# Performance work log

Hardware: AMD Instinct MI355X
Metric: run time of the kernel (lower is better)

## Reference

```python
import jax, jax.numpy as jnp
import numpy as np


def setup_inputs() -> dict:
    key = jax.random.key(0)
    kx, ky = jax.random.split(key)
    x = jax.random.normal(kx, (16, 4096, 3), dtype=jnp.float32)
    y = jax.random.normal(ky, (16, 4096, 3), dtype=jnp.float32)
    return {"x": x, "y": y}


def reference(x, y):
    # avoiding the O(b*N*M*d) difference tensor of the naive expansion.
    x2 = jnp.sum(x * x, axis=-1)                  # (b, N)
    y2 = jnp.sum(y * y, axis=-1)                  # (b, M)
    xy = jnp.einsum('bnd,bmd->bnm', x, y)         # (b, N, M)
    dist = x2[:, :, None] + y2[:, None, :] - 2.0 * xy
    min_d = jnp.min(dist, axis=2)                 # top-1 smallest over M -> (b, N)
    chamfer = jnp.sum(min_d, axis=1) / x.shape[1] # (b,)
    return jnp.sum(chamfer)
```

## Files before the change

### kernel.cpp

```cpp
#include <hip/hip_runtime.h>


constexpr int NPTS    = 4096;
constexpr int NBATCH  = 16;
constexpr int BLOCK   = 256;
constexpr int XPT     = 4;
constexpr int XCHUNK  = BLOCK * XPT;
constexpr int YTILE   = 512;
constexpr int NXC     = NPTS / XCHUNK;
constexpr int NYC     = NPTS / YTILE;

__global__ __launch_bounds__(BLOCK) void chamfer_min_kernel(
    const float* __restrict__ x, const float* __restrict__ y,
    unsigned int* __restrict__ ws_min)
{
    __shared__ float4 sy4[YTILE * 3 / 4];

    const int b      = blockIdx.x >> 5;
    const int xchunk = (blockIdx.x >> 3) & (NXC - 1);
    const int ychunk = blockIdx.x & (NYC - 1);

    const float4* yb4 = (const float4*)(y + ((size_t)b * NPTS + ychunk * YTILE) * 3);
    for (int i = threadIdx.x; i < YTILE * 3 / 4; i += BLOCK) sy4[i] = yb4[i];

    const int xbase = xchunk * XCHUNK + threadIdx.x * XPT;
    const float4* xp4 = (const float4*)(x + ((size_t)b * NPTS + xbase) * 3);
    const float4 a0 = xp4[0], a1 = xp4[1], a2 = xp4[2];
    const float xa[XPT][3] = {
        {a0.x, a0.y, a0.z}, {a0.w, a1.x, a1.y},
        {a1.z, a1.w, a2.x}, {a2.y, a2.z, a2.w}};

    __syncthreads();

    float m[XPT];
    #pragma unroll
    for (int i = 0; i < XPT; ++i) m[i] = 3.4e38f;

    #pragma unroll 2
    for (int j = 0; j < YTILE / 4; ++j) {
        const float4 p = sy4[3 * j + 0];
        const float4 q = sy4[3 * j + 1];
        const float4 r = sy4[3 * j + 2];
        const float ya[4][3] = {
            {p.x, p.y, p.z}, {p.w, q.x, q.y},
            {q.z, q.w, r.x}, {r.y, r.z, r.w}};
        #pragma unroll
        for (int k = 0; k < 4; ++k) {
            #pragma unroll
            for (int i = 0; i < XPT; ++i) {
                const float d0 = xa[i][0] - ya[k][0];
                const float d1 = xa[i][1] - ya[k][1];
                const float d2 = xa[i][2] - ya[k][2];
                const float d  = fmaf(d2, d2, fmaf(d1, d1, d0 * d0));
                m[i] = fminf(m[i], d);
            }
        }
    }

    unsigned int* wm = ws_min + (size_t)b * NPTS + xbase;
    #pragma unroll
    for (int i = 0; i < XPT; ++i)
        atomicMin(&wm[i], __float_as_uint(m[i]));
}

__global__ __launch_bounds__(BLOCK) void chamfer_sum_kernel(
    const unsigned int* __restrict__ ws_min, float* __restrict__ out)
{
    __shared__ float swsum[BLOCK / 64];
    const int total = NBATCH * NPTS;
    float s = 0.f;
    for (int i = blockIdx.x * BLOCK + threadIdx.x; i < total;
         i += gridDim.x * BLOCK)
        s += __uint_as_float(ws_min[i]);

    for (int off = 32; off > 0; off >>= 1)
        s += __shfl_down(s, off, 64);
    const int wave = threadIdx.x >> 6;
    if ((threadIdx.x & 63) == 0) swsum[wave] = s;
    __syncthreads();
    if (threadIdx.x == 0) {
        float t = 0.f;
        #pragma unroll
        for (int w = 0; w < BLOCK / 64; ++w) t += swsum[w];
        atomicAdd(out, t * (1.0f / NPTS));
    }
}

extern "C" void kernel_launch(void* const* d_in, const int* in_sizes, int n_in,
                              void* d_out, int out_size, void* d_ws, size_t ws_size,
                              hipStream_t stream) {
    const float* x = (const float*)d_in[0];
    const float* y = (const float*)d_in[1];
    float* out = (float*)d_out;
    unsigned int* ws_min = (unsigned int*)d_ws;

    hipMemsetAsync(ws_min, 0xFF, (size_t)NBATCH * NPTS * sizeof(unsigned int), stream);
    hipMemsetAsync(out, 0, sizeof(float), stream);

    const int grid1 = NBATCH * NXC * NYC;
    chamfer_min_kernel<<<grid1, BLOCK, 0, stream>>>(x, y, ws_min);
    chamfer_sum_kernel<<<64, BLOCK, 0, stream>>>(ws_min, out);
}
```

Before: 93.38 us.

## Fuse min and sum into a cooperative kernel with an expanded-distance inner loop

Merges the memsets, the min kernel and the sum kernel into one cooperative kernel. Workspace init, the atomicMin merge and the final reduction are separated by grid-wide syncs. The inner loop now uses the ||x||^2+||y||^2-2x.y expansion, with -2y and ||y||^2 precomputed into shared float4s. Each pair then costs three FMAs plus a min instead of subtractions and squares. Each thread also handles 8 x points against 256-point y tiles, which changes occupancy and reuse; the grid syncs and signed-int atomicMin on possibly negative floats add overhead and a small numerical risk.

```diff
diff --git a/kernel.cpp b/kernel.cpp
--- a/kernel.cpp
+++ b/kernel.cpp
@@ -1,34 +1,53 @@
 #include <hip/hip_runtime.h>
+#include <hip/hip_cooperative_groups.h>
+
+namespace cg = cooperative_groups;
 
 
-constexpr int NPTS    = 4096;
-constexpr int NBATCH  = 16;
-constexpr int BLOCK   = 256;
-constexpr int XPT     = 4;
-constexpr int XCHUNK  = BLOCK * XPT;
-constexpr int YTILE   = 512;
-constexpr int NXC     = NPTS / XCHUNK;
-constexpr int NYC     = NPTS / YTILE;
+constexpr int NPTS   = 4096;
+constexpr int NBATCH = 16;
+constexpr int BLOCK  = 256;
+constexpr int XPT    = 8;
+constexpr int XCHUNK = BLOCK * XPT;
+constexpr int NXC    = NPTS / XCHUNK;
+constexpr int YTILE  = 256;
+constexpr int NYC    = NPTS / YTILE;
+constexpr int NBLK   = NBATCH * NXC * NYC;
+constexpr int TOTX   = NBATCH * NPTS;
 
-__global__ __launch_bounds__(BLOCK) void chamfer_min_kernel(
+__global__ __launch_bounds__(BLOCK, 2) void chamfer_fused(
     const float* __restrict__ x, const float* __restrict__ y,
-    unsigned int* __restrict__ ws_min)
+    int* __restrict__ ws_min, float* __restrict__ out)
 {
-    __shared__ float4 sy4[YTILE * 3 / 4];
+    cg::grid_group grid = cg::this_grid();
+    __shared__ float4 syt[YTILE];
+    __shared__ float swsum[BLOCK / 64];
 
-    const int b      = blockIdx.x >> 5;
-    const int xchunk = (blockIdx.x >> 3) & (NXC - 1);
-    const int ychunk = blockIdx.x & (NYC - 1);
+    const int b  = blockIdx.x >> 5;
+    const int xc = (blockIdx.x >> 4) & (NXC - 1);
+    const int yc = blockIdx.x & (NYC - 1);
 
-    const float4* yb4 = (const float4*)(y + ((size_t)b * NPTS + ychunk * YTILE) * 3);
-    for (int i = threadIdx.x; i < YTILE * 3 / 4; i += BLOCK) sy4[i] = yb4[i];
+    const int gx_base = b * NPTS + xc * XCHUNK;
+    const int my_base = gx_base + threadIdx.x * XPT;
 
-    const int xbase = xchunk * XCHUNK + threadIdx.x * XPT;
-    const float4* xp4 = (const float4*)(x + ((size_t)b * NPTS + xbase) * 3);
-    const float4 a0 = xp4[0], a1 = xp4[1], a2 = xp4[2];
-    const float xa[XPT][3] = {
-        {a0.x, a0.y, a0.z}, {a0.w, a1.x, a1.y},
-        {a1.z, a1.w, a2.x}, {a2.y, a2.z, a2.w}};
+    #pragma unroll
+    for (int i = 0; i < XPT; ++i) ws_min[my_base + i] = 0x7FFFFFFF;
+    if (blockIdx.x == 0 && threadIdx.x == 0) out[0] = 0.0f;
+
+    {
+        const float* yp = y + ((size_t)b * NPTS + yc * YTILE + threadIdx.x) * 3;
+        const float y0 = yp[0], y1 = yp[1], y2 = yp[2];
+        syt[threadIdx.x] = make_float4(-2.f * y0, -2.f * y1, -2.f * y2,
+                                       fmaf(y0, y0, fmaf(y1, y1, y2 * y2)));
+    }
+
+    const float4* xp4 = (const float4*)(x + ((size_t)b * NPTS + xc * XCHUNK
+                                             + threadIdx.x * XPT) * 3);
+    const float4 v0 = xp4[0], v1 = xp4[1], v2 = xp4[2],
+                 v3 = xp4[3], v4 = xp4[4], v5 = xp4[5];
+    const float xx[XPT] = {v0.x, v0.w, v1.z, v2.y, v3.x, v3.w, v4.z, v5.y};
+    const float xy[XPT] = {v0.y, v1.x, v1.w, v2.z, v3.y, v4.x, v4.w, v5.z};
+    const float xz[XPT] = {v0.z, v1.y, v2.x, v2.w, v3.z, v4.y, v5.x, v5.w};
 
     __syncthreads();
 
@@ -36,53 +55,45 @@
     #pragma unroll
     for (int i = 0; i < XPT; ++i) m[i] = 3.4e38f;
 
-    #pragma unroll 2
-    for (int j = 0; j < YTILE / 4; ++j) {
-        const float4 p = sy4[3 * j + 0];
-        const float4 q = sy4[3 * j + 1];
-        const float4 r = sy4[3 * j + 2];
-        const float ya[4][3] = {
-            {p.x, p.y, p.z}, {p.w, q.x, q.y},
-            {q.z, q.w, r.x}, {r.y, r.z, r.w}};
+    #pragma unroll 4
+    for (int j = 0; j < YTILE; ++j) {
+        const float4 q = syt[j];
         #pragma unroll
-        for (int k = 0; k < 4; ++k) {
-            #pragma unroll
-            for (int i = 0; i < XPT; ++i) {
-                const float d0 = xa[i][0] - ya[k][0];
-                const float d1 = xa[i][1] - ya[k][1];
-                const float d2 = xa[i][2] - ya[k][2];
-                const float d  = fmaf(d2, d2, fmaf(d1, d1, d0 * d0));
-                m[i] = fminf(m[i], d);
-            }
+        for (int i = 0; i < XPT; ++i) {
+            const float e = fmaf(xx[i], q.x,
+                             fmaf(xy[i], q.y,
+                              fmaf(xz[i], q.z, q.w)));
+            m[i] = fminf(m[i], e);
         }
     }
 
-    unsigned int* wm = ws_min + (size_t)b * NPTS + xbase;
+    __threadfence();
+    grid.sync();
+
     #pragma unroll
-    for (int i = 0; i < XPT; ++i)
-        atomicMin(&wm[i], __float_as_uint(m[i]));
-}
+    for (int i = 0; i < XPT; ++i) {
+        const float x2 = fmaf(xx[i], xx[i],
+                          fmaf(xy[i], xy[i], xz[i] * xz[i]));
+        atomicMin(&ws_min[my_base + i], __float_as_int(m[i] + x2));
+    }
 
-__global__ __launch_bounds__(BLOCK) void chamfer_sum_kernel(
-    const unsigned int* __restrict__ ws_min, float* __restrict__ out)
-{
-    __shared__ float swsum[BLOCK / 64];
-    const int total = NBATCH * NPTS;
-    float s = 0.f;
-    for (int i = blockIdx.x * BLOCK + threadIdx.x; i < total;
-         i += gridDim.x * BLOCK)
-        s += __uint_as_float(ws_min[i]);
+    __threadfence();
+    grid.sync();
 
-    for (int off = 32; off > 0; off >>= 1)
-        s += __shfl_down(s, off, 64);
-    const int wave = threadIdx.x >> 6;
-    if ((threadIdx.x & 63) == 0) swsum[wave] = s;
-    __syncthreads();
-    if (threadIdx.x == 0) {
-        float t = 0.f;
-        #pragma unroll
-        for (int w = 0; w < BLOCK / 64; ++w) t += swsum[w];
-        atomicAdd(out, t * (1.0f / NPTS));
+    if (blockIdx.x < TOTX / BLOCK) {
+        const int gx = blockIdx.x * BLOCK + threadIdx.x;
+        float s = __int_as_float(ws_min[gx]);
+        for (int off = 32; off > 0; off >>= 1)
+            s += __shfl_down(s, off, 64);
+        const int wave = threadIdx.x >> 6;
+        if ((threadIdx.x & 63) == 0) swsum[wave] = s;
+        __syncthreads();
+        if (threadIdx.x == 0) {
+            float t = 0.f;
+            #pragma unroll
+            for (int w = 0; w < BLOCK / 64; ++w) t += swsum[w];
+            atomicAdd(out, t * (1.0f / NPTS));
+        }
     }
 }
 
@@ -92,12 +103,9 @@
     const float* x = (const float*)d_in[0];
     const float* y = (const float*)d_in[1];
     float* out = (float*)d_out;
-    unsigned int* ws_min = (unsigned int*)d_ws;
+    int* ws_min = (int*)d_ws;
 
-    hipMemsetAsync(ws_min, 0xFF, (size_t)NBATCH * NPTS * sizeof(unsigned int), stream);
-    hipMemsetAsync(out, 0, sizeof(float), stream);
-
-    const int grid1 = NBATCH * NXC * NYC;
-    chamfer_min_kernel<<<grid1, BLOCK, 0, stream>>>(x, y, ws_min);
-    chamfer_sum_kernel<<<64, BLOCK, 0, stream>>>(ws_min, out);
+    void* args[] = {(void*)&x, (void*)&y, (void*)&ws_min, (void*)&out};
+    hipLaunchCooperativeKernel((void*)chamfer_fused, dim3(NBLK), dim3(BLOCK),
+                               args, 0, stream);
 }
```

After: 236.2 us. 153% more time.
